# Performance work log

Hardware: AMD Instinct MI355X
Metric: run time of the kernel (lower is better)

## Reference

```python
import jax, jax.numpy as jnp
import numpy as np
import math

HEADS = 8
DIM_HEAD = 64


def setup_inputs() -> dict:
    key = jax.random.key(0)
    k1, k2, k3 = jax.random.split(key, 3)
    b, n, dim = 4, 2048, 512
    inner = HEADS * DIM_HEAD  # 512
    x = jax.random.normal(k1, (b, n, dim), dtype=jnp.float32)
    W_qkv = jax.random.normal(k2, (dim, 4 * inner), dtype=jnp.float32) * (dim ** -0.5)
    W_out = jax.random.normal(k3, (2 * inner, dim), dtype=jnp.float32) * ((2 * inner) ** -0.5)
    b_out = jnp.zeros((dim,), dtype=jnp.float32)
    return {"x": x, "W_qkv": W_qkv, "W_out": W_out, "b_out": b_out}


def reference(x, W_qkv, W_out, b_out):
    b, n, d = x.shape
    h, dh = HEADS, DIM_HEAD
    scale = dh ** -0.5
    qkvt = x @ W_qkv  # [b, n, 4*h*dh]
    q, k, v, t = jnp.split(qkvt, 4, axis=-1)
    # 'b n (h d) -> b h n d'
    def to_heads(z):
        return z.reshape(b, n, h, dh).transpose(0, 2, 1, 3)
    q, k, v, t = map(to_heads, (q, k, v, t))

    # Branch 1: standard softmax attention
    dots = jnp.einsum('bhid,bhjd->bhij', q, k) * scale
    attn1 = jax.nn.softmax(dots, axis=-1)
    out1 = jnp.einsum('bhij,bhjd->bhid', attn1, v)

    # Branch 2: fixed positional-decay attention (shared across b, h; no repeat needed)
    pos = jnp.arange(1, n + 1, dtype=x.dtype)  # linspace(1, n, n)
    tg = jnp.abs(pos[None, :] - pos[:, None])  # |j - i|, [n, n]
    attn2 = jnp.exp(-tg / jnp.asarray(math.e, dtype=x.dtype))
    # NOTE: original divides by sum(-1) WITHOUT keepdim -> broadcasts over columns:
    # attn2[i, j] / sum_k attn2[j, k]
    attn2 = attn2 / attn2.sum(-1)
    out2 = jnp.einsum('ij,bhjd->bhid', attn2, t)

    out = jnp.concatenate([out1, out2], axis=-1)  # [b, h, n, 2*dh]
    out = out.transpose(0, 2, 1, 3).reshape(b, n, 2 * h * dh)  # 'b h n d -> b n (h d)'
    return out @ W_out + b_out
```

## Files before the change

### kernel.cpp

```cpp
#include <hip/hip_runtime.h>
#include <hip/hip_bf16.h>

#define B_ 4
#define N_ 2048
#define D_ 512
#define H_ 8
#define DH_ 64

typedef float float4_ __attribute__((ext_vector_type(4)));
typedef int int2_ __attribute__((ext_vector_type(2)));
typedef int int4_ __attribute__((ext_vector_type(4)));
typedef unsigned short ushort4_ __attribute__((ext_vector_type(4)));
typedef unsigned short ushort8_ __attribute__((ext_vector_type(8)));
typedef __bf16 bf16x8 __attribute__((ext_vector_type(8)));
typedef _Float16 half2_ __attribute__((ext_vector_type(2)));
typedef _Float16 half4_ __attribute__((ext_vector_type(4)));
typedef _Float16 half8_ __attribute__((ext_vector_type(8)));

#if __has_builtin(__builtin_amdgcn_exp2f)
#define EXP2(x) __builtin_amdgcn_exp2f(x)
#else
#define EXP2(x) exp2f(x)
#endif

__device__ __forceinline__ float b2f(unsigned short u) {
  union { unsigned int u; float f; } v; v.u = ((unsigned int)u) << 16; return v.f;
}
__device__ __forceinline__ unsigned short f2b(float f) {
  union { float f; unsigned int u; } v; v.f = f;
  unsigned int r = v.u + 0x7fffu + ((v.u >> 16) & 1u);
  return (unsigned short)(r >> 16);
}
__device__ __forceinline__ half4_ pk4(float a, float b, float c, float d) {
  half2_ lo = __builtin_bit_cast(half2_, __builtin_amdgcn_cvt_pkrtz(a, b));
  half2_ hi = __builtin_bit_cast(half2_, __builtin_amdgcn_cvt_pkrtz(c, d));
  return __builtin_bit_cast(half4_,
      (int2_){__builtin_bit_cast(int, lo), __builtin_bit_cast(int, hi)});
}

#define GLD16(gp, lp)                                                        \
  __builtin_amdgcn_global_load_lds(                                          \
      (const __attribute__((address_space(1))) unsigned int*)(gp),           \
      (__attribute__((address_space(3))) unsigned int*)(lp), 16, 0, 0)

__device__ __forceinline__ bool detect_fp32_local(
    const unsigned short* __restrict__ xhdr, int* cnt_sh) {
  if (threadIdx.x == 0) *cnt_sh = 0;
  __syncthreads();
  unsigned int e = (xhdr[threadIdx.x] >> 7) & 0xFFu;
  if (e >= 134u) atomicAdd(cnt_sh, 1);
  __syncthreads();
  return *cnt_sh > 16;
}

__device__ __forceinline__ void transpose_conv(
    const void* __restrict__ src, unsigned short* __restrict__ dst,
    int R, int C, int bx, int by, bool ofp) {
  __shared__ unsigned short tile[32][33];
  const int c0 = bx * 32, r0 = by * 32;
  const int tx = threadIdx.x & 31, ty = threadIdx.x >> 5;
#pragma unroll
  for (int k = 0; k < 4; ++k) {
    int r = ty + k * 8;
    long idx = (long)(r0 + r) * C + c0 + tx;
    tile[r][tx] = ofp ? f2b(((const float*)src)[idx])
                      : ((const unsigned short*)src)[idx];
  }
  __syncthreads();
#pragma unroll
  for (int k = 0; k < 4; ++k) {
    int c = ty + k * 8;
    dst[(long)(c0 + c) * R + r0 + tx] = tile[tx][c];
  }
}

__global__ __launch_bounds__(256) void prep_all(
    const void* __restrict__ xraw, const void* __restrict__ Wqraw,
    const void* __restrict__ Woraw, unsigned short* __restrict__ xb,
    unsigned short* __restrict__ WqT, unsigned short* __restrict__ WoT,
    unsigned short* __restrict__ Wband) {
  __shared__ int cnt_sh;
  const bool ofp = detect_fp32_local((const unsigned short*)xraw, &cnt_sh);
  const int bid = blockIdx.x;
  if (bid < 4096) {
    int i4 = bid * 256 + threadIdx.x;
    ushort4_ o;
    if (ofp) {
      float4_ v = ((const float4_*)xraw)[i4];
      o[0] = f2b(v[0]); o[1] = f2b(v[1]); o[2] = f2b(v[2]); o[3] = f2b(v[3]);
    } else {
      o = ((const ushort4_*)xraw)[i4];
    }
    *(ushort4_*)(xb + (long)i4 * 4) = o;
  } else if (bid < 5120) {
    const int b2 = bid - 4096;
    transpose_conv(Wqraw, WqT, 512, 2048, b2 % 64, b2 / 64, ofp);
  } else if (bid < 5632) {
    const int b2 = bid - 5120;
    transpose_conv(Woraw, WoT, 1024, 512, b2 % 16, b2 / 16, ofp);
  } else {
    constexpr float INV_E = 0.36787944117144233f;
    constexpr float R1 = 0.69220062755534635f;
    constexpr float INV_1MR = 3.2488706f;
    const int i = bid - 5632;
    const int krel = threadIdx.x;
    const int j = (i >> 6) * 64 - 96 + krel;
    float c = 0.f;
    if (j >= 0 && j < N_) {
      float wgt = __expf(-fabsf((float)(i - j)) * INV_E);
      float rj = __expf(-(float)j * INV_E);
      float rnj = __expf(-(float)(N_ - 1 - j) * INV_E);
      float S = 1.f + R1 * (2.f - rj - rnj) * INV_1MR;
      c = wgt / S;
    }
    _Float16 hv = (_Float16)c;
    Wband[i * 256 + krel] = __builtin_bit_cast(unsigned short, hv);
  }
}

__global__ __launch_bounds__(256) void gemm128(
    const unsigned short* __restrict__ A, const unsigned short* __restrict__ Bt,
    unsigned short* __restrict__ C, int M, int N, int K) {
  __shared__ unsigned short As[128 * 32];
  __shared__ unsigned short Bs[128 * 32];
  const int tid = threadIdx.x;
  const int w = tid >> 6, lane = tid & 63, l16 = lane & 15, quad = lane >> 4;
  const int wm = (w & 1) * 64, wn = (w >> 1) * 64;
  const long tm = (long)blockIdx.x * 128, tn = (long)blockIdx.y * 128;
  const int srow = w * 32 + (lane >> 2);
  const int scol = (lane & 3) * 8;
  float4_ acc[4][4] = {};
  for (int k0 = 0; k0 < K; k0 += 32) {
#pragma unroll
    for (int q = 0; q < 2; ++q) {
      GLD16(&A[(tm + srow + q * 16) * K + k0 + scol], &As[(w * 32 + q * 16) * 32]);
      GLD16(&Bt[(tn + srow + q * 16) * K + k0 + scol], &Bs[(w * 32 + q * 16) * 32]);
    }
    __syncthreads();
    bf16x8 af[4], bf[4];
#pragma unroll
    for (int mb = 0; mb < 4; ++mb)
      af[mb] = __builtin_bit_cast(bf16x8,
          *(const int4_*)&As[(wm + mb * 16 + l16) * 32 + quad * 8]);
#pragma unroll
    for (int nb = 0; nb < 4; ++nb)
      bf[nb] = __builtin_bit_cast(bf16x8,
          *(const int4_*)&Bs[(wn + nb * 16 + l16) * 32 + quad * 8]);
#pragma unroll
    for (int mb = 0; mb < 4; ++mb)
#pragma unroll
      for (int nb = 0; nb < 4; ++nb)
        acc[mb][nb] = __builtin_amdgcn_mfma_f32_16x16x32_bf16(
            af[mb], bf[nb], acc[mb][nb], 0, 0, 0);
    __syncthreads();
  }
#pragma unroll
  for (int nb = 0; nb < 4; ++nb) {
    long col = tn + wn + nb * 16 + l16;
#pragma unroll
    for (int mb = 0; mb < 4; ++mb)
#pragma unroll
      for (int r = 0; r < 4; ++r) {
        long row = tm + wm + mb * 16 + quad * 4 + r;
        C[row * N + col] = f2b(acc[mb][nb][r]);
      }
  }
}

__global__ __launch_bounds__(256) void gemm_n64(
    const unsigned short* __restrict__ A, const unsigned short* __restrict__ Bt,
    void* __restrict__ C, const void* __restrict__ bias_raw,
    int M, int N, int K, const unsigned short* __restrict__ xhdr) {
  __shared__ int cnt_sh;
  const bool ofp = detect_fp32_local(xhdr, &cnt_sh);
  __shared__ unsigned short As[128 * 32];
  __shared__ unsigned short Bs[64 * 32];
  const int tid = threadIdx.x;
  const int w = tid >> 6, lane = tid & 63, l16 = lane & 15, quad = lane >> 4;
  const int wm = (w & 1) * 64, wn = (w >> 1) * 32;
  const long tm = (long)blockIdx.x * 128, tn = (long)blockIdx.y * 64;
  const int srowA = w * 32 + (lane >> 2);
  const int srowB = w * 16 + (lane >> 2);
  const int scol = (lane & 3) * 8;
  float4_ acc[4][2] = {};
  for (int k0 = 0; k0 < K; k0 += 32) {
#pragma unroll
    for (int q = 0; q < 2; ++q)
      GLD16(&A[(tm + srowA + q * 16) * K + k0 + scol], &As[(w * 32 + q * 16) * 32]);
    GLD16(&Bt[(tn + srowB) * K + k0 + scol], &Bs[(w * 16) * 32]);
    __syncthreads();
    bf16x8 af[4], bf[2];
#pragma unroll
    for (int mb = 0; mb < 4; ++mb)
      af[mb] = __builtin_bit_cast(bf16x8,
          *(const int4_*)&As[(wm + mb * 16 + l16) * 32 + quad * 8]);
#pragma unroll
    for (int nb = 0; nb < 2; ++nb)
      bf[nb] = __builtin_bit_cast(bf16x8,
          *(const int4_*)&Bs[(wn + nb * 16 + l16) * 32 + quad * 8]);
#pragma unroll
    for (int mb = 0; mb < 4; ++mb)
#pragma unroll
      for (int nb = 0; nb < 2; ++nb)
        acc[mb][nb] = __builtin_amdgcn_mfma_f32_16x16x32_bf16(
            af[mb], bf[nb], acc[mb][nb], 0, 0, 0);
    __syncthreads();
  }
#pragma unroll
  for (int nb = 0; nb < 2; ++nb) {
    long col = tn + wn + nb * 16 + l16;
    float bv = ofp ? ((const float*)bias_raw)[col]
                   : b2f(((const unsigned short*)bias_raw)[col]);
#pragma unroll
    for (int mb = 0; mb < 4; ++mb)
#pragma unroll
      for (int r = 0; r < 4; ++r) {
        long row = tm + wm + mb * 16 + quad * 4 + r;
        float val = acc[mb][nb][r] + bv;
        if (ofp) ((float*)C)[row * N + col] = val;
        else ((unsigned short*)C)[row * N + col] = f2b(val);
      }
  }
}

#define TSW 266
__global__ __launch_bounds__(256) void mid_all(
    const unsigned short* __restrict__ qkvt, unsigned short* __restrict__ Vt,
    const unsigned short* __restrict__ Wband, unsigned short* __restrict__ catb) {
  __shared__ unsigned short Ts[64 * TSW];
  const int bid = blockIdx.x;
  const int tid = threadIdx.x;
  if (bid < 4096) {
    unsigned short (*tile)[33] = (unsigned short (*)[33])Ts;
    const int j0 = (bid & 63) * 32;
    const int bh = (bid >> 6) & 31, b = bh >> 3, h = bh & 7;
    const int d0 = (bid >> 11) * 32;
    const int tx = tid & 31, ty = tid >> 5;
#pragma unroll
    for (int k = 0; k < 4; ++k) {
      int j = ty + k * 8;
      tile[j][tx] = qkvt[(long)(b * N_ + j0 + j) * 2048 + 1024 + h * 64 + d0 + tx];
    }
    __syncthreads();
#pragma unroll
    for (int k = 0; k < 4; ++k) {
      int dd = ty + k * 8;
      _Float16 hv = (_Float16)b2f(tile[tx][dd]);
      Vt[((long)bh * 64 + d0 + dd) * 2048 + j0 + tx] =
          __builtin_bit_cast(unsigned short, hv);
    }
    return;
  }
  const int b2 = bid - 4096;
  const int qtile = b2 & 31;
  const int bh = b2 >> 5, b = bh >> 3, h = bh & 7;
  const int jlo = qtile * 64 - 96;
  {
    const int d = tid & 63;
    const int kkb = tid >> 6;
#pragma unroll
    for (int it = 0; it < 64; ++it) {
      const int kk = it * 4 + kkb;
      const int j = jlo + kk;
      unsigned short us = 0;
      if (j >= 0 && j < N_) {
        _Float16 hv = (_Float16)b2f(qkvt[(long)(b * N_ + j) * 2048 + 1536 + h * 64 + d]);
        us = __builtin_bit_cast(unsigned short, hv);
      }
      Ts[d * TSW + kk] = us;
    }
  }
  __syncthreads();
  const int w = tid >> 6, lane = tid & 63, l16 = lane & 15, quad = lane >> 4;
  const int i_row = qtile * 64 + w * 16 + l16;
  const unsigned short* ap = Wband + i_row * 256;
  float4_ acc[4] = {};
#pragma unroll
  for (int kh = 0; kh < 8; ++kh) {
    half8_ af = __builtin_bit_cast(half8_, *(const int4_*)&ap[kh * 32 + quad * 8]);
#pragma unroll
    for (int nb = 0; nb < 4; ++nb) {
      half8_ bf = __builtin_bit_cast(half8_,
          *(const int4_*)&Ts[(nb * 16 + l16) * TSW + kh * 32 + quad * 8]);
      acc[nb] = __builtin_amdgcn_mfma_f32_16x16x32_f16(af, bf, acc[nb], 0, 0, 0);
    }
  }
#pragma unroll
  for (int nb = 0; nb < 4; ++nb)
#pragma unroll
    for (int r = 0; r < 4; ++r) {
      int row = qtile * 64 + w * 16 + quad * 4 + r;
      catb[(long)(b * N_ + row) * 1024 + h * 128 + 64 + nb * 16 + l16] =
          f2b(acc[nb][r]);
    }
}

__global__ __launch_bounds__(256) void flash_kernel(
    const unsigned short* __restrict__ qkvt, const unsigned short* __restrict__ Vt,
    unsigned short* __restrict__ catb) {
  __shared__ unsigned short Ks[2][64 * 64];
  __shared__ unsigned short Vs[2][64 * 64];
  const int bh = blockIdx.y, b = bh >> 3, h = bh & 7;
  const int i0 = blockIdx.x * 64;
  const int tid = threadIdx.x;
  const int w = tid >> 6, lane = tid & 63, l16 = lane & 15, quad = lane >> 4;
  const int srow8 = lane >> 3, sch = lane & 7;
  const int chK = sch ^ srow8;
  bf16x8 qf[2];
  {
    constexpr float SCL = 0.125f * 1.44269504088896f;
    const long qrow = (long)(b * N_ + i0 + w * 16 + l16) * 2048 + h * 64;
#pragma unroll
    for (int kh = 0; kh < 2; ++kh) {
      ushort8_ raw = __builtin_bit_cast(ushort8_,
          *(const int4_*)&qkvt[qrow + kh * 32 + quad * 8]);
      ushort8_ sc;
#pragma unroll
      for (int e = 0; e < 8; ++e) sc[e] = f2b(b2f(raw[e]) * SCL);
      qf[kh] = __builtin_bit_cast(bf16x8, sc);
    }
  }
  const unsigned short* kp[2];
#pragma unroll
  for (int kh = 0; kh < 2; ++kh)
    kp[kh] = &Ks[0][l16 * 64 + (((kh * 4 + quad) ^ (l16 & 7)) * 8)];
  const unsigned short* vp[4];
#pragma unroll
  for (int c = 0; c < 4; ++c)
    vp[c] = &Vs[0][l16 * 64 + (((c * 2 + (quad >> 1)) ^ (l16 & 7)) * 8) +
                   (quad & 1) * 4];
  const unsigned short* kg[2];
  const unsigned short* vg[2];
#pragma unroll
  for (int g = 0; g < 2; ++g) {
    const int row = w * 16 + g * 8 + srow8;
    kg[g] = qkvt + (long)(b * N_ + row) * 2048 + 512 + h * 64 + chK * 8;
    vg[g] = Vt + ((long)bh * 64 + row) * 2048 + chK * 8;
  }
  float4_ O[4] = {};
  float4_ O5 = {};
  const half4_ ones = {(_Float16)1.f, (_Float16)1.f, (_Float16)1.f, (_Float16)1.f};

  auto stage = [&](int jt_, int buf_) __attribute__((always_inline)) {
    const int j0 = jt_ * 64;
#pragma unroll
    for (int g = 0; g < 2; ++g) {
      GLD16(kg[g] + (long)j0 * 2048,
            (char*)&Ks[0][0] + buf_ * 8192 + (w * 16 + g * 8) * 128);
      GLD16(vg[g] + j0,
            (char*)&Vs[0][0] + buf_ * 8192 + (w * 16 + g * 8) * 128);
    }
  };
  auto phase = [&](int jt_, int buf_) __attribute__((always_inline)) {
    if (jt_ + 1 < 32) stage(jt_ + 1, buf_ ^ 1);
    float4_ s[4] = {};
#pragma unroll
    for (int kh = 0; kh < 2; ++kh)
#pragma unroll
      for (int c = 0; c < 4; ++c) {
        bf16x8 kf = __builtin_bit_cast(bf16x8,
            *(const int4_*)(kp[kh] + buf_ * 4096 + c * 1024));
        s[c] = __builtin_amdgcn_mfma_f32_16x16x32_bf16(kf, qf[kh], s[c], 0, 0, 0);
      }
    half4_ pf[4];
#pragma unroll
    for (int c = 0; c < 4; ++c)
      pf[c] = pk4(EXP2(s[c][0]), EXP2(s[c][1]), EXP2(s[c][2]), EXP2(s[c][3]));
#pragma unroll
    for (int c = 0; c < 4; ++c) {
#pragma unroll
      for (int dblk = 0; dblk < 4; ++dblk) {
        half4_ vfv = *(const half4_*)(vp[c] + buf_ * 4096 + dblk * 1024);
        O[dblk] = __builtin_amdgcn_mfma_f32_16x16x16f16(
            pf[c], vfv, O[dblk], 0, 0, 0);
      }
      O5 = __builtin_amdgcn_mfma_f32_16x16x16f16(pf[c], ones, O5, 0, 0, 0);
    }
    __syncthreads();
  };

  stage(0, 0);
  __syncthreads();
  for (int jt = 0; jt < 32; jt += 2) {
    phase(jt, 0);
    phase(jt + 1, 1);
  }
  float linv[4];
#pragma unroll
  for (int r = 0; r < 4; ++r) linv[r] = 1.f / O5[r];
#pragma unroll
  for (int dblk = 0; dblk < 4; ++dblk)
#pragma unroll
    for (int r = 0; r < 4; ++r) {
      int row = i0 + w * 16 + quad * 4 + r;
      catb[(long)(b * N_ + row) * 1024 + h * 128 + dblk * 16 + l16] =
          f2b(O[dblk][r] * linv[r]);
    }
}

extern "C" void kernel_launch(void* const* d_in, const int* in_sizes, int n_in,
                              void* d_out, int out_size, void* d_ws, size_t ws_size,
                              hipStream_t stream) {
  char* ws = (char*)d_ws;
  unsigned short* qkvt = (unsigned short*)(ws);
  unsigned short* WqT  = (unsigned short*)(ws + (size_t)32 * 1024 * 1024);
  unsigned short* WoT  = (unsigned short*)(ws + (size_t)34 * 1024 * 1024);
  unsigned short* Vt   = (unsigned short*)(ws + (size_t)35 * 1024 * 1024);
  unsigned short* catb = (unsigned short*)(ws + (size_t)43 * 1024 * 1024);
  unsigned short* xb   = (unsigned short*)(ws + (size_t)59 * 1024 * 1024);
  unsigned short* Wband= (unsigned short*)(ws + (size_t)68 * 1024 * 1024);

  prep_all<<<7680, 256, 0, stream>>>(d_in[0], d_in[1], d_in[2],
                                     xb, WqT, WoT, Wband);
  gemm128<<<dim3(8192 / 128, 2048 / 128), 256, 0, stream>>>(
      xb, WqT, qkvt, 8192, 2048, 512);
  mid_all<<<5120, 256, 0, stream>>>(qkvt, Vt, Wband, catb);
  flash_kernel<<<dim3(2048 / 64, 32), 256, 0, stream>>>(qkvt, Vt, catb);
  gemm_n64<<<dim3(8192 / 128, 512 / 64), 256, 0, stream>>>(
      catb, WoT, d_out, d_in[3], 8192, 512, 1024,
      (const unsigned short*)d_in[0]);
}
```

Before: 211.3 us.

## Replace QKV GEMM with 256x256 double-buffered, swizzled 8-wave MFMA kernel

The 128x128 single-buffered QKV projection GEMM is replaced by a 256x256-tile kernel with 512 threads, double-buffered LDS staging of 64-wide K slices, and XOR-swizzled LDS addressing. Each iteration splits the MFMA work into four quadrant phases interleaved with LDS reads and the global prefetch of the next tile, using s_setprio to favor MFMA issue. The aim is more data reuse per tile, hiding global load latency, and avoiding LDS bank conflicts. In exchange it uses 128KB of LDS per block and gives a grid of only 256 blocks, which limits occupancy.

```diff
diff --git a/kernel.cpp b/kernel.cpp
--- a/kernel.cpp
+++ b/kernel.cpp
@@ -118,51 +118,141 @@
   }
 }
 
-__global__ __launch_bounds__(256) void gemm128(
+#define MFMA16x32(d, a, b) \
+  d = __builtin_amdgcn_mfma_f32_16x16x32_bf16(a, b, d, 0, 0, 0)
+
+__global__ __launch_bounds__(512, 2) void gemm256(
     const unsigned short* __restrict__ A, const unsigned short* __restrict__ Bt,
     unsigned short* __restrict__ C, int M, int N, int K) {
-  __shared__ unsigned short As[128 * 32];
-  __shared__ unsigned short Bs[128 * 32];
+  __shared__ unsigned short As[2][16384];
+  __shared__ unsigned short Bs[2][16384];
   const int tid = threadIdx.x;
   const int w = tid >> 6, lane = tid & 63, l16 = lane & 15, quad = lane >> 4;
-  const int wm = (w & 1) * 64, wn = (w >> 1) * 64;
-  const long tm = (long)blockIdx.x * 128, tn = (long)blockIdx.y * 128;
-  const int srow = w * 32 + (lane >> 2);
-  const int scol = (lane & 3) * 8;
-  float4_ acc[4][4] = {};
-  for (int k0 = 0; k0 < K; k0 += 32) {
-#pragma unroll
-    for (int q = 0; q < 2; ++q) {
-      GLD16(&A[(tm + srow + q * 16) * K + k0 + scol], &As[(w * 32 + q * 16) * 32]);
-      GLD16(&Bt[(tn + srow + q * 16) * K + k0 + scol], &Bs[(w * 32 + q * 16) * 32]);
-    }
-    __syncthreads();
-    bf16x8 af[4], bf[4];
-#pragma unroll
-    for (int mb = 0; mb < 4; ++mb)
-      af[mb] = __builtin_bit_cast(bf16x8,
-          *(const int4_*)&As[(wm + mb * 16 + l16) * 32 + quad * 8]);
-#pragma unroll
-    for (int nb = 0; nb < 4; ++nb)
-      bf[nb] = __builtin_bit_cast(bf16x8,
-          *(const int4_*)&Bs[(wn + nb * 16 + l16) * 32 + quad * 8]);
-#pragma unroll
-    for (int mb = 0; mb < 4; ++mb)
-#pragma unroll
-      for (int nb = 0; nb < 4; ++nb)
-        acc[mb][nb] = __builtin_amdgcn_mfma_f32_16x16x32_bf16(
-            af[mb], bf[nb], acc[mb][nb], 0, 0, 0);
-    __syncthreads();
-  }
-#pragma unroll
-  for (int nb = 0; nb < 4; ++nb) {
-    long col = tn + wn + nb * 16 + l16;
-#pragma unroll
-    for (int mb = 0; mb < 4; ++mb)
+  const int wm = w >> 2, wn = w & 3;
+  const long tm = (long)blockIdx.x * 256, tn = (long)blockIdx.y * 256;
+
+  const int srow = tid >> 3;
+  const int sch = (tid & 7) ^ (srow & 7);
+  const unsigned short* gA = A + (tm + srow) * (long)K + sch * 8;
+  const unsigned short* gB = Bt + (tn + srow) * (long)K + sch * 8;
+
+  const int xr8 = l16 & 7;
+  const int ch0 = ((0 + quad) ^ xr8) * 8;
+  const int ch1 = ((4 + quad) ^ xr8) * 8;
+  const int rowA0 = (wm * 128 + l16) * 64;
+  const int rowB0 = (wn * 64 + l16) * 64;
+
+  float4_ acc[8][4] = {};
+
+  auto stage = [&](int t, int bufn) __attribute__((always_inline)) {
+#pragma unroll
+    for (int r = 0; r < 4; ++r)
+      GLD16(gA + (long)(r * 64) * K + t * 64, &As[bufn][r * 4096 + w * 512]);
+#pragma unroll
+    for (int r = 0; r < 4; ++r)
+      GLD16(gB + (long)(r * 64) * K + t * 64, &Bs[bufn][r * 4096 + w * 512]);
+  };
+
+  stage(0, 0);
+  asm volatile("s_waitcnt vmcnt(0)" ::: "memory");
+  __builtin_amdgcn_s_barrier();
+
+  const int NT = K >> 6;
+  for (int t = 0; t < NT; ++t) {
+    const int buf = t & 1;
+    const unsigned short* as = As[buf];
+    const unsigned short* bs = Bs[buf];
+    bf16x8 af[8], bq[4], br[4];
+#pragma unroll
+    for (int mi = 0; mi < 4; ++mi) {
+      af[mi * 2]     = __builtin_bit_cast(bf16x8, *(const int4_*)&as[rowA0 + mi * 1024 + ch0]);
+      af[mi * 2 + 1] = __builtin_bit_cast(bf16x8, *(const int4_*)&as[rowA0 + mi * 1024 + ch1]);
+    }
+#pragma unroll
+    for (int ni = 0; ni < 2; ++ni) {
+      bq[ni * 2]     = __builtin_bit_cast(bf16x8, *(const int4_*)&bs[rowB0 + ni * 1024 + ch0]);
+      bq[ni * 2 + 1] = __builtin_bit_cast(bf16x8, *(const int4_*)&bs[rowB0 + ni * 1024 + ch1]);
+    }
+    if (t + 1 < NT) stage(t + 1, buf ^ 1);
+    __builtin_amdgcn_s_barrier();
+    asm volatile("s_waitcnt lgkmcnt(0)" ::: "memory");
+    __builtin_amdgcn_sched_barrier(0);
+    __builtin_amdgcn_s_setprio(1);
+#pragma unroll
+    for (int mi = 0; mi < 4; ++mi)
+#pragma unroll
+      for (int ni = 0; ni < 2; ++ni) {
+        MFMA16x32(acc[mi][ni], af[mi * 2], bq[ni * 2]);
+        MFMA16x32(acc[mi][ni], af[mi * 2 + 1], bq[ni * 2 + 1]);
+      }
+    __builtin_amdgcn_s_setprio(0);
+    __builtin_amdgcn_s_barrier();
+#pragma unroll
+    for (int ni = 0; ni < 2; ++ni) {
+      br[ni * 2]     = __builtin_bit_cast(bf16x8, *(const int4_*)&bs[rowB0 + (2 + ni) * 1024 + ch0]);
+      br[ni * 2 + 1] = __builtin_bit_cast(bf16x8, *(const int4_*)&bs[rowB0 + (2 + ni) * 1024 + ch1]);
+    }
+    __builtin_amdgcn_s_barrier();
+    asm volatile("s_waitcnt lgkmcnt(0)" ::: "memory");
+    __builtin_amdgcn_sched_barrier(0);
+    __builtin_amdgcn_s_setprio(1);
+#pragma unroll
+    for (int mi = 0; mi < 4; ++mi)
+#pragma unroll
+      for (int ni = 0; ni < 2; ++ni) {
+        MFMA16x32(acc[mi][2 + ni], af[mi * 2], br[ni * 2]);
+        MFMA16x32(acc[mi][2 + ni], af[mi * 2 + 1], br[ni * 2 + 1]);
+      }
+    __builtin_amdgcn_s_setprio(0);
+    __builtin_amdgcn_s_barrier();
+#pragma unroll
+    for (int mi = 0; mi < 4; ++mi) {
+      af[mi * 2]     = __builtin_bit_cast(bf16x8, *(const int4_*)&as[rowA0 + (4 + mi) * 1024 + ch0]);
+      af[mi * 2 + 1] = __builtin_bit_cast(bf16x8, *(const int4_*)&as[rowA0 + (4 + mi) * 1024 + ch1]);
+    }
+    __builtin_amdgcn_s_barrier();
+    asm volatile("s_waitcnt lgkmcnt(0)" ::: "memory");
+    __builtin_amdgcn_sched_barrier(0);
+    __builtin_amdgcn_s_setprio(1);
+#pragma unroll
+    for (int mi = 0; mi < 4; ++mi)
+#pragma unroll
+      for (int ni = 0; ni < 2; ++ni) {
+        MFMA16x32(acc[4 + mi][2 + ni], af[mi * 2], br[ni * 2]);
+        MFMA16x32(acc[4 + mi][2 + ni], af[mi * 2 + 1], br[ni * 2 + 1]);
+      }
+    __builtin_amdgcn_s_setprio(0);
+    __builtin_amdgcn_s_barrier();
+#pragma unroll
+    for (int ni = 0; ni < 2; ++ni) {
+      bq[ni * 2]     = __builtin_bit_cast(bf16x8, *(const int4_*)&bs[rowB0 + ni * 1024 + ch0]);
+      bq[ni * 2 + 1] = __builtin_bit_cast(bf16x8, *(const int4_*)&bs[rowB0 + ni * 1024 + ch1]);
+    }
+    __builtin_amdgcn_s_barrier();
+    asm volatile("s_waitcnt lgkmcnt(0)" ::: "memory");
+    __builtin_amdgcn_sched_barrier(0);
+    __builtin_amdgcn_s_setprio(1);
+#pragma unroll
+    for (int mi = 0; mi < 4; ++mi)
+#pragma unroll
+      for (int ni = 0; ni < 2; ++ni) {
+        MFMA16x32(acc[4 + mi][ni], af[mi * 2], bq[ni * 2]);
+        MFMA16x32(acc[4 + mi][ni], af[mi * 2 + 1], bq[ni * 2 + 1]);
+      }
+    __builtin_amdgcn_s_setprio(0);
+    asm volatile("s_waitcnt vmcnt(0)" ::: "memory");
+    __builtin_amdgcn_sched_barrier(0);
+    __builtin_amdgcn_s_barrier();
+  }
+#pragma unroll
+  for (int ni = 0; ni < 4; ++ni) {
+    long col = tn + wn * 64 + ni * 16 + l16;
+#pragma unroll
+    for (int mi = 0; mi < 8; ++mi)
 #pragma unroll
       for (int r = 0; r < 4; ++r) {
-        long row = tm + wm + mb * 16 + quad * 4 + r;
-        C[row * N + col] = f2b(acc[mb][nb][r]);
+        long row = tm + wm * 128 + mi * 16 + quad * 4 + r;
+        C[row * N + col] = f2b(acc[mi][ni][r]);
       }
   }
 }
@@ -412,7 +502,7 @@
 
   prep_all<<<7680, 256, 0, stream>>>(d_in[0], d_in[1], d_in[2],
                                      xb, WqT, WoT, Wband);
-  gemm128<<<dim3(8192 / 128, 2048 / 128), 256, 0, stream>>>(
+  gemm256<<<dim3(8192 / 256, 2048 / 256), 512, 0, stream>>>(
       xb, WqT, qkvt, 8192, 2048, 512);
   mid_all<<<5120, 256, 0, stream>>>(qkvt, Vt, Wband, catb);
   flash_kernel<<<dim3(2048 / 64, 32), 256, 0, stream>>>(qkvt, Vt, catb);
```

New measurement: 207.8 us. About the same (-1.7%).
